# Performance work log

Hardware: AMD Instinct MI355X
Metric: run time of the kernel (lower is better)

## Reference

```python
import math
import jax, jax.numpy as jnp
import numpy as np

B, C, H, W = 8, 256, 32, 32
NH, DK, DV = 8, 32, 32
EPS = 1e-6


def mish(x):
    return x * jnp.tanh(jax.nn.softplus(x))


def grouped_conv1x1(x, w, b, groups):
    # x: (B, Cin, N); w: (Cout, Cin//groups); b: (Cout,)
    Bb, Cin, N = x.shape
    Cout = w.shape[0]
    xg = x.reshape(Bb, groups, Cin // groups, N)
    wg = w.reshape(groups, Cout // groups, Cin // groups)
    y = jnp.einsum('bgin,goi->bgon', xg, wg).reshape(Bb, Cout, N)
    return y + b[None, :, None]


def conv_block(x, w, b, s, beta, groups):
    # 1x1 conv -> BatchNorm (eval: running mean 0 / var 1 => affine) -> Mish
    y = grouped_conv1x1(x, w, b, groups)
    y = s[None, :, None] * y + beta[None, :, None]
    return mish(y)


def setup_inputs() -> dict:
    key = jax.random.key(0)
    ks = jax.random.split(key, 8)
    inp = {
        'x': jax.random.normal(ks[0], (B, C, H, W), dtype=jnp.float32),
        'q_w': jax.random.normal(ks[1], (NH * DK, C // NH), dtype=jnp.float32) * 0.05,
        'q_b': jnp.zeros((NH * DK,), jnp.float32),
        'q_s': jnp.ones((NH * DK,), jnp.float32),
        'q_beta': jnp.zeros((NH * DK,), jnp.float32),
        'k_w': jax.random.normal(ks[2], (NH * DK, C // NH), dtype=jnp.float32) * 0.05,
        'k_b': jnp.zeros((NH * DK,), jnp.float32),
        'k_s': jnp.ones((NH * DK,), jnp.float32),
        'k_beta': jnp.zeros((NH * DK,), jnp.float32),
        'v_w': jax.random.normal(ks[3], (NH * DV, C // NH), dtype=jnp.float32) * 0.05,
        'v_b': jnp.zeros((NH * DV,), jnp.float32),
        'v_s': jnp.ones((NH * DV,), jnp.float32),
        'v_beta': jnp.zeros((NH * DV,), jnp.float32),
        'f_w': jax.random.normal(ks[4], (C, NH * DV), dtype=jnp.float32) * 0.05,
        'f_b': jnp.zeros((C,), jnp.float32),
        'f_s': jnp.ones((C,), jnp.float32),
        'f_beta': jnp.zeros((C,), jnp.float32),
    }
    return inp


def _forward(x, q_w, q_b, q_s, q_beta, k_w, k_b, k_s, k_beta,
             v_w, v_b, v_s, v_beta, f_w, f_b, f_s, f_beta):
    b, c, h, w = x.shape
    n = h * w
    temp = math.sqrt(c / NH)
    xf = x.reshape(b, c, n)

    q = conv_block(xf, q_w, q_b, q_s, q_beta, NH).reshape(b, NH, DK, n) / temp
    k = conv_block(xf, k_w, k_b, k_s, k_beta, NH).reshape(b, NH, DK, n)
    v = conv_block(xf, v_w, v_b, v_s, v_beta, NH).reshape(b, NH, DV, n)

    # cosine-distance attention (all heads vectorized); identical math to the
    # torch broadcast/repeat version but computed via normalized dot products.
    qn = jnp.sqrt(jnp.sum(q * q, axis=2))  # (b, nh, n)
    kn = jnp.sqrt(jnp.sum(k * k, axis=2))
    dot = jnp.einsum('bhdn,bhdm->bhnm', q, k)  # (b, nh, n, n)
    denom = jnp.maximum(qn[:, :, :, None] * kn[:, :, None, :], EPS)
    cos = jnp.clip(dot / denom, -1.0 + 1e-6, 1.0 - 1e-6)
    attn = jax.nn.softmax(1.0 - jnp.arccos(cos) / math.pi, axis=-1)

    # out[..., d, i] = sum_m v[..., d, m] * attn[..., i, m]
    out = jnp.einsum('bhdm,bhnm->bhdn', v, attn).reshape(b, NH * DV, n)

    y = conv_block(out, f_w, f_b, f_s, f_beta, 1).reshape(b, c, h, w) + x

    # extract_attn_map (no_grad in original)
    am = jnp.sum(jnp.mean(attn, axis=1), axis=1)  # (b, n)
    mn = jnp.min(am, axis=1, keepdims=True)
    mx = jnp.max(am, axis=1, keepdims=True)
    am = ((am - mn) / (mx - mn)).reshape(b, h, w)
    return y, jax.lax.stop_gradient(am)


def reference(x, q_w, q_b, q_s, q_beta, k_w, k_b, k_s, k_beta,
              v_w, v_b, v_s, v_beta, f_w, f_b, f_s, f_beta):
    return _forward(x, q_w, q_b, q_s, q_beta, k_w, k_b, k_s, k_beta,
                    v_w, v_b, v_s, v_beta, f_w, f_b, f_s, f_beta)
```

## Files before the change

kernel.cpp:

```cpp
#include <hip/hip_runtime.h>
#include <math.h>

#define B_   8
#define C_   256
#define NH_  8
#define N_   1024
#define LOG2E    1.4426950408889634f

typedef __attribute__((ext_vector_type(8))) short bf16x8;
typedef __attribute__((ext_vector_type(4))) float f32x4;
typedef __attribute__((ext_vector_type(2))) float f32x2;
typedef unsigned short u16;
typedef unsigned int u32;

#define AS1 __attribute__((address_space(1)))
#define AS3 __attribute__((address_space(3)))

__device__ __forceinline__ f32x4 mfma16(bf16x8 a, bf16x8 b, f32x4 c) {
    return __builtin_amdgcn_mfma_f32_16x16x32_bf16(a, b, c, 0, 0, 0);
}
__device__ __forceinline__ u32 bf16r(float x) {
    u32 b = __float_as_uint(x);
    return (b + 0x7fffu + ((b >> 16) & 1u)) >> 16;
}
__device__ __forceinline__ float mish_fast(float x) {
    float e  = __builtin_amdgcn_exp2f(fminf(x, 30.f) * LOG2E);
    float nm = e * (e + 2.f);
    return x * nm * __builtin_amdgcn_rcpf(nm + 2.f);
}
__device__ __forceinline__ f32x2 splat2(float v) { return (f32x2){v, v}; }
__device__ __forceinline__ f32x2 fexp_poly2(f32x2 c) {
    c = __builtin_elementwise_min(
            __builtin_elementwise_max(c, splat2(-0.999999f)), splat2(0.999999f));
    f32x2 r = __builtin_elementwise_fma(splat2(6.3713280f), c, splat2(1.7809920f));
    r = __builtin_elementwise_fma(r, c, splat2(-15.1427584f));
    r = __builtin_elementwise_fma(r, c, splat2(-3.7571968f));
    r = __builtin_elementwise_fma(r, c, splat2(13.1518784f));
    r = __builtin_elementwise_fma(r, c, splat2(2.8140000f));
    r = __builtin_elementwise_fma(r, c, splat2(-4.8903712f));
    r = __builtin_elementwise_fma(r, c, splat2(-0.8122592f));
    r = __builtin_elementwise_fma(r, c, splat2(0.8441120f));
    r = __builtin_elementwise_fma(r, c, splat2(0.1705120f));
    r = __builtin_elementwise_fma(r, c, splat2(0.4936541f));
    r = __builtin_elementwise_fma(r, c, splat2(1.6473155f));
    return r;
}

__global__ __launch_bounds__(256) void qkvpack_kernel(
    const float* __restrict__ x,
    const float* __restrict__ qw, const float* __restrict__ qb2,
    const float* __restrict__ qs, const float* __restrict__ qbeta,
    const float* __restrict__ kw, const float* __restrict__ kb2,
    const float* __restrict__ ks, const float* __restrict__ kbeta,
    const float* __restrict__ vw, const float* __restrict__ vb2,
    const float* __restrict__ vs, const float* __restrict__ vbeta,
    uint4* __restrict__ qpk, uint4* __restrict__ kpk, u16* __restrict__ vbf,
    const float* __restrict__ fw, u16* __restrict__ wbf)
{
    int blk = blockIdx.x;
    if (blk >= 768) {
        int id = (blk - 768) * 1024 + threadIdx.x;
#pragma unroll
        for (int j = 0; j < 4; ++j) { int p = id + j * 256; wbf[p] = (u16)bf16r(fw[p]); }
        return;
    }
    int type = blk >> 8;
    int sub = blk & 255;
    int nt = sub & 3, g = (sub >> 2) & 7, b = sub >> 5;
    int n = nt * 256 + threadIdx.x;
    int bh = b * 8 + g;
    const float* xp = x + ((size_t)b * C_ + g * 32) * N_ + n;
    float xv[32];
#pragma unroll
    for (int i = 0; i < 32; ++i) xv[i] = xp[(size_t)i * N_];

    const float *w, *bb, *sc, *bt;
    if (type == 0)      { w = qw; bb = qb2; sc = qs; bt = qbeta; }
    else if (type == 1) { w = kw; bb = kb2; sc = ks; bt = kbeta; }
    else                { w = vw; bb = vb2; sc = vs; bt = vbeta; }

    float y[32];
#pragma unroll
    for (int co = 0; co < 32; ++co) {
        int cg = g * 32 + co;
        float acc = 0.f;
#pragma unroll
        for (int i = 0; i < 32; ++i)
            acc = fmaf(xv[i], w[cg * 32 + i], acc);
        y[co] = mish_fast(sc[cg] * (acc + bb[cg]) + bt[cg]);
    }

    if (type == 2) {
#pragma unroll
        for (int co = 0; co < 32; ++co)
            vbf[((size_t)bh * 32 + co) * N_ + n] = (u16)bf16r(y[co]);
        return;
    }
    float s2 = 0.f;
#pragma unroll
    for (int d = 0; d < 32; ++d) s2 = fmaf(y[d], y[d], s2);
    float inv = __builtin_amdgcn_rsqf(fmaxf(s2, 1e-24f));
    u32 wp[16];
#pragma unroll
    for (int d = 0; d < 16; ++d)
        wp[d] = bf16r(y[2 * d] * inv) | (bf16r(y[2 * d + 1] * inv) << 16);
    uint4* dst = (type == 0 ? qpk : kpk) + ((size_t)bh * N_ + n) * 4;
#pragma unroll
    for (int j = 0; j < 4; ++j)
        dst[j] = make_uint4(wp[4 * j], wp[4 * j + 1], wp[4 * j + 2], wp[4 * j + 3]);
}

__global__ __launch_bounds__(256) void attn_kernel(
    const u16* __restrict__ qpk, const u16* __restrict__ kpk,
    const u16* __restrict__ vbf,
    u16* __restrict__ aout_bt, float* __restrict__ ampart)
{
    __shared__ __align__(16) u16 Kc[4][128][8];
    __shared__ __align__(16) u16 Vc[32][128];
    __shared__ __align__(16) u16 Ps[4][16 * 136];
    __shared__ __align__(16) float amW[N_];

    const int tid  = threadIdx.x;
    const int wave = tid >> 6, lane = tid & 63;
    const int l15 = lane & 15, lg = lane >> 4;
    const int blk = blockIdx.x;
    const int itile = blk & 15, bh = blk >> 4;
    const int h = bh & 7, bidx = bh >> 3;
    const int i0 = itile * 64;

    const char* ksrc = (const char*)(kpk + (size_t)bh * N_ * 32);
    const char* vsrc = (const char*)(vbf + (size_t)bh * 32 * N_);
    const char* qsrc = (const char*)(qpk + (size_t)bh * N_ * 32);

    for (int j = tid; j < N_; j += 256) amW[j] = 0.f;

    bf16x8 aq = *(const bf16x8*)(qsrc + (size_t)(i0 + wave * 16 + l15) * 64 + lg * 16);

    const char* kfb = (const char*)Kc + lg * 2048 + l15 * 16;

    f32x2 rsL = {0.f, 0.f}, rsH = {0.f, 0.f};
    for (int ch = 0; ch < 8; ++ch) {
        int m0 = ch * 128;
        __syncthreads();
#pragma unroll
        for (int p = 0; p < 2; ++p) {
            int gi = p * 256 + wave * 64 + lane;
            int j = gi >> 7, m = gi & 127;
            __builtin_amdgcn_global_load_lds(
                (const AS1 void*)(ksrc + (size_t)(m0 + m) * 64 + j * 16),
                (AS3 void*)((char*)Kc + ((p * 256 + wave * 64) << 4)), 16, 0, 0);
        }
        __syncthreads();
#pragma unroll
        for (int t = 0; t < 8; ++t) {
            bf16x8 bk = *(const bf16x8*)(kfb + t * 256);
            f32x4 cf = {0.f, 0.f, 0.f, 0.f};
            cf = mfma16(aq, bk, cf);
            rsL += fexp_poly2((f32x2){cf[0], cf[1]});
            rsH += fexp_poly2((f32x2){cf[2], cf[3]});
        }
    }
    float rinv[4];
    {
        float rr[4] = {rsL.x, rsL.y, rsH.x, rsH.y};
#pragma unroll
        for (int r = 0; r < 4; ++r) {
            float s = rr[r];
            s += __shfl_xor(s, 1); s += __shfl_xor(s, 2);
            s += __shfl_xor(s, 4); s += __shfl_xor(s, 8);
            rinv[r] = __builtin_amdgcn_rcpf(s);
        }
    }
    f32x2 rinvL = {rinv[0], rinv[1]}, rinvH = {rinv[2], rinv[3]};

    f32x4 o0 = {0.f, 0.f, 0.f, 0.f}, o1 = {0.f, 0.f, 0.f, 0.f};
    char*       psw = (char*)&Ps[wave][0] + lg * 1088 + l15 * 2;
    const char* pab = (const char*)&Ps[wave][0] + l15 * 272 + lg * 16;
    const char* vfb = (const char*)Vc + l15 * 256;
    const int   vkey = l15 & 7;

    for (int ch = 0; ch < 8; ++ch) {
        int m0 = ch * 128;
        __syncthreads();
#pragma unroll
        for (int p = 0; p < 2; ++p) {
            int gi = p * 256 + wave * 64 + lane;
            int j = gi >> 7, m = gi & 127;
            __builtin_amdgcn_global_load_lds(
                (const AS1 void*)(ksrc + (size_t)(m0 + m) * 64 + j * 16),
                (AS3 void*)((char*)Kc + ((p * 256 + wave * 64) << 4)), 16, 0, 0);
        }
#pragma unroll
        for (int p = 0; p < 2; ++p) {
            int gi = p * 256 + wave * 64 + lane;
            int d = gi >> 4, gm = gi & 15;
            __builtin_amdgcn_global_load_lds(
                (const AS1 void*)(vsrc + (size_t)d * 2048 + m0 * 2 + ((gm ^ (d & 7)) << 4)),
                (AS3 void*)((char*)Vc + ((p * 256 + wave * 64) << 4)), 16, 0, 0);
        }
        __syncthreads();

#pragma unroll
        for (int t = 0; t < 8; ++t) {
            bf16x8 bk = *(const bf16x8*)(kfb + t * 256);
            f32x4 cf = {0.f, 0.f, 0.f, 0.f};
            cf = mfma16(aq, bk, cf);
            f32x2 fL = fexp_poly2((f32x2){cf[0], cf[1]});
            f32x2 fH = fexp_poly2((f32x2){cf[2], cf[3]});
            *(u16*)(psw + 0 * 272 + t * 32) = (u16)bf16r(fL.x);
            *(u16*)(psw + 1 * 272 + t * 32) = (u16)bf16r(fL.y);
            *(u16*)(psw + 2 * 272 + t * 32) = (u16)bf16r(fH.x);
            *(u16*)(psw + 3 * 272 + t * 32) = (u16)bf16r(fH.y);
            f32x2 cs2 = fL * rinvL;
            cs2 = __builtin_elementwise_fma(fH, rinvH, cs2);
            float csum = cs2.x + cs2.y;
            csum += __shfl_xor(csum, 16);
            csum += __shfl_xor(csum, 32);
            if (lane < 16) atomicAdd(&amW[m0 + t * 16 + l15], csum);
        }
        asm volatile("s_waitcnt lgkmcnt(0)" ::: "memory");
        __builtin_amdgcn_sched_barrier(0);
#pragma unroll
        for (int kss = 0; kss < 4; ++kss) {
            bf16x8 pa = *(const bf16x8*)(pab + kss * 64);
            const char* va = vfb + (((kss * 4 + lg) ^ vkey) << 4);
            bf16x8 v0 = *(const bf16x8*)va;
            bf16x8 v1 = *(const bf16x8*)(va + 4096);
            o0 = mfma16(pa, v0, o0);
            o1 = mfma16(pa, v1, o1);
        }
    }
    __syncthreads();

    {
        u16* oT = (u16*)Ps;
#pragma unroll
        for (int r = 0; r < 4; ++r) {
            int irow = wave * 16 + lg * 4 + r;
            oT[irow * 40 + l15]      = (u16)bf16r(o0[r] * rinv[r]);
            oT[irow * 40 + 16 + l15] = (u16)bf16r(o1[r] * rinv[r]);
        }
    }
    __syncthreads();
    {
        const u16* oT = (const u16*)Ps;
        int row = tid >> 2, c4 = tid & 3;
        uint4 val = *(const uint4*)((const char*)oT + row * 80 + c4 * 16);
        int n = i0 + row;
        int g = h * 4 + c4;
        size_t dst = ((size_t)(bidx * N_ + n) << 9) + ((size_t)((g ^ (row & 7)) << 4));
        *(uint4*)((char*)aout_bt + dst) = val;
    }
#pragma unroll
    for (int j2 = 0; j2 < 4; ++j2)
        ampart[(size_t)blk * N_ + tid + 256 * j2] = amW[tid + 256 * j2];
}

__global__ __launch_bounds__(256) void fconv_kernel(
    const u16* __restrict__ aout_bt, const u16* __restrict__ wbf,
    const float* __restrict__ x,
    const float* __restrict__ fs, const float* __restrict__ fb,
    const float* __restrict__ fbeta, float* __restrict__ y,
    const float* __restrict__ ampart, float* __restrict__ outAm)
{
    __shared__ __align__(16) u16 As[32 * 256];
    __shared__ float rmn[256], rmx[256];
    const int tid = threadIdx.x;

    if (blockIdx.x >= 256) {
        int b = blockIdx.x - 256;
        const float* base = ampart + (size_t)b * 128 * N_;
        float s[4] = {0.f, 0.f, 0.f, 0.f};
        for (int p = 0; p < 128; ++p) {
#pragma unroll
            for (int c2 = 0; c2 < 4; ++c2)
                s[c2] += base[(size_t)p * N_ + tid + 256 * c2];
        }
        float mn = fminf(fminf(s[0], s[1]), fminf(s[2], s[3]));
        float mx = fmaxf(fmaxf(s[0], s[1]), fmaxf(s[2], s[3]));
        rmn[tid] = mn; rmx[tid] = mx;
        __syncthreads();
        for (int off = 128; off >= 1; off >>= 1) {
            if (tid < off) {
                rmn[tid] = fminf(rmn[tid], rmn[tid + off]);
                rmx[tid] = fmaxf(rmx[tid], rmx[tid + off]);
            }
            __syncthreads();
        }
        mn = rmn[0]; mx = rmx[0];
        float inv = 1.f / (mx - mn);
#pragma unroll
        for (int c2 = 0; c2 < 4; ++c2)
            outAm[(size_t)b * N_ + tid + 256 * c2] = (s[c2] - mn) * inv;
        return;
    }

    const int wave = tid >> 6, lane = tid & 63;
    const int l15 = lane & 15, lg = lane >> 4;
    const int b  = blockIdx.x >> 5;
    const int n0 = (blockIdx.x & 31) * 32;

    const char* asrc = (const char*)aout_bt + ((size_t)(b * N_ + n0) << 9);
#pragma unroll
    for (int p = 0; p < 4; ++p) {
        int g = p * 256 + wave * 64 + lane;
        __builtin_amdgcn_global_load_lds(
            (const AS1 void*)(asrc + g * 16),
            (AS3 void*)((char*)As + ((p * 256 + wave * 64) << 4)), 16, 0, 0);
    }
    __syncthreads();

    f32x4 acc[4][2];
#pragma unroll
    for (int f = 0; f < 4; ++f)
#pragma unroll
        for (int fn = 0; fn < 2; ++fn) acc[f][fn] = (f32x4){0.f, 0.f, 0.f, 0.f};

    const int cobase = wave * 64;
#pragma unroll
    for (int kk = 0; kk < 8; ++kk) {
        bf16x8 af[2];
#pragma unroll
        for (int fn = 0; fn < 2; ++fn) {
            int nf = fn * 16 + l15;
            af[fn] = *(const bf16x8*)((const char*)As + nf * 512 +
                                      (((kk * 4 + lg) ^ (nf & 7)) << 4));
        }
#pragma unroll
        for (int f = 0; f < 4; ++f) {
            bf16x8 wf = *(const bf16x8*)(wbf + (size_t)(cobase + f * 16 + l15) * 256 + kk * 32 + lg * 8);
            acc[f][0] = mfma16(wf, af[0], acc[f][0]);
            acc[f][1] = mfma16(wf, af[1], acc[f][1]);
        }
    }

#pragma unroll
    for (int f = 0; f < 4; ++f) {
#pragma unroll
        for (int r = 0; r < 4; ++r) {
            int co = cobase + f * 16 + lg * 4 + r;
            float sc = fs[co], bb = fb[co], bt = fbeta[co];
#pragma unroll
            for (int fn = 0; fn < 2; ++fn) {
                int n = n0 + fn * 16 + l15;
                size_t oid = ((size_t)(b * C_ + co) << 10) + n;
                y[oid] = mish_fast(sc * (acc[f][fn][r] + bb) + bt) + x[oid];
            }
        }
    }
}

extern "C" void kernel_launch(void* const* d_in, const int* in_sizes, int n_in,
                              void* d_out, int out_size, void* d_ws, size_t ws_size,
                              hipStream_t stream)
{
    const float* x     = (const float*)d_in[0];
    const float* q_w   = (const float*)d_in[1];
    const float* q_b   = (const float*)d_in[2];
    const float* q_s   = (const float*)d_in[3];
    const float* q_be  = (const float*)d_in[4];
    const float* k_w   = (const float*)d_in[5];
    const float* k_b   = (const float*)d_in[6];
    const float* k_s   = (const float*)d_in[7];
    const float* k_be  = (const float*)d_in[8];
    const float* v_w   = (const float*)d_in[9];
    const float* v_b   = (const float*)d_in[10];
    const float* v_s   = (const float*)d_in[11];
    const float* v_be  = (const float*)d_in[12];
    const float* f_w   = (const float*)d_in[13];
    const float* f_b   = (const float*)d_in[14];
    const float* f_s   = (const float*)d_in[15];
    const float* f_be  = (const float*)d_in[16];

    float* y_out  = (float*)d_out;
    float* am_out = (float*)d_out + (size_t)B_ * C_ * N_;

    char* w = (char*)d_ws;
    u16*   qpk     = (u16*)w;    w += (size_t)B_ * NH_ * N_ * 64;
    u16*   kpk     = (u16*)w;    w += (size_t)B_ * NH_ * N_ * 64;
    u16*   vbf     = (u16*)w;    w += (size_t)B_ * C_ * N_ * 2;
    u16*   aout_bt = (u16*)w;    w += (size_t)B_ * N_ * C_ * 2;
    float* ampart  = (float*)w;  w += (size_t)B_ * NH_ * 16 * N_ * 4;
    u16*   wbf     = (u16*)w;

    qkvpack_kernel<<<832, 256, 0, stream>>>(
        x, q_w, q_b, q_s, q_be, k_w, k_b, k_s, k_be,
        v_w, v_b, v_s, v_be, (uint4*)qpk, (uint4*)kpk, vbf, f_w, wbf);

    attn_kernel<<<B_ * NH_ * 16, 256, 0, stream>>>(
        qpk, kpk, vbf, aout_bt, ampart);

    fconv_kernel<<<264, 256, 0, stream>>>(
        aout_bt, wbf, x, f_s, f_b, f_be, y_out, ampart, am_out);
}
```

Baseline: 107.3 us.

## Read K and V fragments directly from global memory instead of LDS staging

After: 119.4 us. +11.3%, slower.

```diff
diff --git a/kernel.cpp b/kernel.cpp
--- a/kernel.cpp
+++ b/kernel.cpp
@@ -115,8 +115,6 @@
     const u16* __restrict__ vbf,
     u16* __restrict__ aout_bt, float* __restrict__ ampart)
 {
-    __shared__ __align__(16) u16 Kc[4][128][8];
-    __shared__ __align__(16) u16 Vc[32][128];
     __shared__ __align__(16) u16 Ps[4][16 * 136];
     __shared__ __align__(16) float amW[N_];
 
@@ -133,32 +131,21 @@
     const char* qsrc = (const char*)(qpk + (size_t)bh * N_ * 32);
 
     for (int j = tid; j < N_; j += 256) amW[j] = 0.f;
+    __syncthreads();
 
     bf16x8 aq = *(const bf16x8*)(qsrc + (size_t)(i0 + wave * 16 + l15) * 64 + lg * 16);
 
-    const char* kfb = (const char*)Kc + lg * 2048 + l15 * 16;
+    const char* kfb = ksrc + l15 * 64 + lg * 16;
+    const char* vfb = vsrc + l15 * 2048 + lg * 16;
 
     f32x2 rsL = {0.f, 0.f}, rsH = {0.f, 0.f};
-    for (int ch = 0; ch < 8; ++ch) {
-        int m0 = ch * 128;
-        __syncthreads();
-#pragma unroll
-        for (int p = 0; p < 2; ++p) {
-            int gi = p * 256 + wave * 64 + lane;
-            int j = gi >> 7, m = gi & 127;
-            __builtin_amdgcn_global_load_lds(
-                (const AS1 void*)(ksrc + (size_t)(m0 + m) * 64 + j * 16),
-                (AS3 void*)((char*)Kc + ((p * 256 + wave * 64) << 4)), 16, 0, 0);
-        }
-        __syncthreads();
-#pragma unroll
-        for (int t = 0; t < 8; ++t) {
-            bf16x8 bk = *(const bf16x8*)(kfb + t * 256);
-            f32x4 cf = {0.f, 0.f, 0.f, 0.f};
-            cf = mfma16(aq, bk, cf);
-            rsL += fexp_poly2((f32x2){cf[0], cf[1]});
-            rsH += fexp_poly2((f32x2){cf[2], cf[3]});
-        }
+#pragma unroll 8
+    for (int t = 0; t < 64; ++t) {
+        bf16x8 bk = *(const bf16x8*)(kfb + t * 1024);
+        f32x4 cf = {0.f, 0.f, 0.f, 0.f};
+        cf = mfma16(aq, bk, cf);
+        rsL += fexp_poly2((f32x2){cf[0], cf[1]});
+        rsH += fexp_poly2((f32x2){cf[2], cf[3]});
     }
     float rinv[4];
     {
@@ -176,33 +163,12 @@
     f32x4 o0 = {0.f, 0.f, 0.f, 0.f}, o1 = {0.f, 0.f, 0.f, 0.f};
     char*       psw = (char*)&Ps[wave][0] + lg * 1088 + l15 * 2;
     const char* pab = (const char*)&Ps[wave][0] + l15 * 272 + lg * 16;
-    const char* vfb = (const char*)Vc + l15 * 256;
-    const int   vkey = l15 & 7;
 
     for (int ch = 0; ch < 8; ++ch) {
         int m0 = ch * 128;
-        __syncthreads();
-#pragma unroll
-        for (int p = 0; p < 2; ++p) {
-            int gi = p * 256 + wave * 64 + lane;
-            int j = gi >> 7, m = gi & 127;
-            __builtin_amdgcn_global_load_lds(
-                (const AS1 void*)(ksrc + (size_t)(m0 + m) * 64 + j * 16),
-                (AS3 void*)((char*)Kc + ((p * 256 + wave * 64) << 4)), 16, 0, 0);
-        }
-#pragma unroll
-        for (int p = 0; p < 2; ++p) {
-            int gi = p * 256 + wave * 64 + lane;
-            int d = gi >> 4, gm = gi & 15;
-            __builtin_amdgcn_global_load_lds(
-                (const AS1 void*)(vsrc + (size_t)d * 2048 + m0 * 2 + ((gm ^ (d & 7)) << 4)),
-                (AS3 void*)((char*)Vc + ((p * 256 + wave * 64) << 4)), 16, 0, 0);
-        }
-        __syncthreads();
-
 #pragma unroll
         for (int t = 0; t < 8; ++t) {
-            bf16x8 bk = *(const bf16x8*)(kfb + t * 256);
+            bf16x8 bk = *(const bf16x8*)(kfb + (m0 + t * 16) * 64);
             f32x4 cf = {0.f, 0.f, 0.f, 0.f};
             cf = mfma16(aq, bk, cf);
             f32x2 fL = fexp_poly2((f32x2){cf[0], cf[1]});
@@ -223,9 +189,9 @@
 #pragma unroll
         for (int kss = 0; kss < 4; ++kss) {
             bf16x8 pa = *(const bf16x8*)(pab + kss * 64);
-            const char* va = vfb + (((kss * 4 + lg) ^ vkey) << 4);
+            const char* va = vfb + (m0 + kss * 32) * 2;
             bf16x8 v0 = *(const bf16x8*)va;
-            bf16x8 v1 = *(const bf16x8*)(va + 4096);
+            bf16x8 v1 = *(const bf16x8*)(va + 32768);
             o0 = mfma16(pa, v0, o0);
             o1 = mfma16(pa, v1, o1);
         }
```
